# Performance work log

Hardware: AMD Instinct MI355X
Metric: run time of the kernel (lower is better)

## Reference

```python
import jax, jax.numpy as jnp
import numpy as np

LAM = 1.0
N_ITERS = 20
TOL = 1e-6


def setup_inputs() -> dict:
    key = jax.random.key(0)
    k0, k1, k2, k3, k4 = jax.random.split(key, 5)
    B, M, d, E, a = 8, 50000, 8, 800000, 8
    c0 = jax.random.normal(k0, (B, M, d), dtype=jnp.float32)
    src = jax.random.randint(k1, (E,), 0, M, dtype=jnp.int32)
    dst = jax.random.randint(k2, (E,), 0, M, dtype=jnp.int32)
    R_src = jax.random.normal(k3, (E, a, d), dtype=jnp.float32)
    R_dst = jax.random.normal(k4, (E, a, d), dtype=jnp.float32)
    return {"c0": c0, "src": src, "dst": dst, "R_src": R_src, "R_dst": R_dst}


def _batch_dot(x, y):
    # [B,M,d] x [B,M,d] -> [B,1,1]
    return jnp.sum(x * y, axis=(1, 2), keepdims=True)


def _matvec(p, src, dst, R_src, R_dst):
    # p: [B,M,d] -> p + lam * L p via per-edge gather-einsum-scatter
    r = (jnp.einsum('ead,bed->bea', R_src, p[:, src, :])
         - jnp.einsum('ead,bed->bea', R_dst, p[:, dst, :]))  # [B,E,a]
    c_src = jnp.einsum('ead,bea->bed', R_src, r)   # [B,E,d]
    c_dst = -jnp.einsum('ead,bea->bed', R_dst, r)  # [B,E,d]
    acc = jnp.zeros_like(p).at[:, src, :].add(c_src).at[:, dst, :].add(c_dst)
    return p + LAM * acc


def _cg_solve(b, x0, src, dst, R_src, R_dst):
    mv = lambda q: _matvec(q, src, dst, R_src, R_dst)
    x = x0
    r = b - mv(x)
    p = r
    rsold = _batch_dot(r, r)
    done = jnp.array(False)

    def body(i, state):
        x, r, p, rsold, done = state
        Ap = mv(p)
        alpha = rsold / (_batch_dot(p, Ap) + 1e-12)
        x_new = x + alpha * p
        r_new = r - alpha * Ap
        rsnew = _batch_dot(r_new, r_new)
        conv = jnp.sqrt(jnp.mean(rsnew)) < TOL  # torch breaks AFTER updating x,r
        p_new = r_new + rsnew / (rsold + 1e-12) * p
        x = jnp.where(done, x, x_new)
        r = jnp.where(done, r, r_new)
        frozen = done | conv
        p = jnp.where(frozen, p, p_new)
        rsold = jnp.where(frozen, rsold, rsnew)
        return (x, r, p, rsold, frozen)

    x, _, _, _, _ = jax.lax.fori_loop(0, N_ITERS, body, (x, r, p, rsold, done))
    return x


def reference(c0, src, dst, R_src, R_dst):
    c0_f = c0.astype(jnp.float32)
    c = _cg_solve(c0_f, c0_f, src, dst, R_src, R_dst)
    return c.astype(c0.dtype)
```

## Files before the change

kernel.cpp:

```cpp
#include <hip/hip_runtime.h>
#include <math.h>

constexpr float LAM = 1.0f;
constexpr int   NIT = 20;
constexpr float TOL = 1e-6f;

typedef float f4 __attribute__((ext_vector_type(4)));

#define S_RSOLD 0
#define S_ALPHA 8
#define S_BETA  16
#define S_FLAG  24
#define S_PAP   32
#define S_RS    (32+2048)
#define SCAL_F  (32+4096)

__device__ __forceinline__ float dot8v(f4 a0, f4 a1, f4 b0, f4 b1){
  return a0[0]*b0[0] + a0[1]*b0[1] + a0[2]*b0[2] + a0[3]*b0[3]
       + a1[0]*b1[0] + a1[1]*b1[1] + a1[2]*b1[2] + a1[3]*b1[3];
}

__global__ void k_setup_nm(float* __restrict__ scal, int* __restrict__ cursor, int Mn){
  int i = blockIdx.x * blockDim.x + threadIdx.x;
  int stride = gridDim.x * blockDim.x;
  for (int j = i; j < SCAL_F; j += stride) scal[j] = 0.f;
  for (int j = i; j < Mn; j += stride) cursor[j] = 0;
}

__global__ void k_deg(const int* __restrict__ src, const int* __restrict__ dst,
                      int* __restrict__ cnt, int E){
  int i = blockIdx.x * blockDim.x + threadIdx.x;
  int stride = gridDim.x * blockDim.x;
  for (int e = i; e < E; e += stride){
    atomicAdd(&cnt[src[e]], 1);
    atomicAdd(&cnt[dst[e]], 1);
  }
}

__global__ void k_scan(int* __restrict__ cnt, int* __restrict__ rowptr,
                       int* __restrict__ cursor, int Mn, int tot){
  __shared__ int sm[1024];
  const int T = 1024;
  int t = threadIdx.x;
  int chunk = (Mn + T - 1) / T;
  int lo = t * chunk, hi = lo + chunk; if (hi > Mn) hi = Mn;
  int s = 0;
  for (int i = lo; i < hi; ++i) s += cnt[i];
  sm[t] = s;
  __syncthreads();
  for (int o = 1; o < T; o <<= 1){
    int v = (t >= o) ? sm[t - o] : 0;
    __syncthreads();
    sm[t] += v;
    __syncthreads();
  }
  int base = (t == 0) ? 0 : sm[t - 1];
  for (int i = lo; i < hi; ++i){
    int c = cnt[i];
    rowptr[i] = base;
    cursor[i] = base;
    base += c;
  }
  if (t == T - 1) rowptr[Mn] = tot;
}

__global__ void k_fill(const int* __restrict__ src, const int* __restrict__ dst,
                       int* __restrict__ cursor, int* __restrict__ col,
                       int* __restrict__ es, int E){
  int i = blockIdx.x * blockDim.x + threadIdx.x;
  int stride = gridDim.x * blockDim.x;
  for (int e = i; e < E; e += stride){
    int s = src[e], t = dst[e];
    int ps = atomicAdd(&cursor[s], 1);
    col[ps] = t; es[ps] = (e << 1);
    int pt = atomicAdd(&cursor[t], 1);
    col[pt] = s; es[pt] = (e << 1) | 1;
  }
}

__global__ void k_medge(const float* __restrict__ Rs, const float* __restrict__ Rd,
                        float* __restrict__ Mb, int E){
  int g  = blockIdx.x * blockDim.x + threadIdx.x;
  int wv = g >> 6, l = g & 63;
  int nw = (gridDim.x * blockDim.x) >> 6;
  int d1 = l >> 3, d2 = l & 7;
  for (int e = wv; e < E; e += nw){
    float rs = Rs[(size_t)e * 64 + l];
    float rd = Rd[(size_t)e * 64 + l];
    float Mm = 0.f;
    #pragma unroll
    for (int a = 0; a < 8; ++a)
      Mm += __shfl(rs, a * 8 + d1, 64) * __shfl(rd, a * 8 + d2, 64);
    Mb[(size_t)e * 64 + l] = Mm;
  }
}

__global__ void k_buildd(const float* __restrict__ Rs, const float* __restrict__ Rd,
                         const int* __restrict__ rowptr, const int* __restrict__ es,
                         float* __restrict__ Dd, int v0, int v1){
  int g = blockIdx.x * blockDim.x + threadIdx.x;
  int v = v0 + (g >> 6);
  if (v >= v1) return;
  int l = g & 63, d1 = l >> 3, d2 = l & 7;
  float Dacc = 0.f;
  int j0 = rowptr[v], j1 = rowptr[v + 1];
  int j = j0;
  for (; j + 2 <= j1; j += 2){
    int e0 = es[j], e1 = es[j + 1];
    const float* R0 = (e0 & 1) ? Rd : Rs;
    const float* R1 = (e1 & 1) ? Rd : Rs;
    float x0 = R0[(size_t)(e0 >> 1) * 64 + l];
    float x1 = R1[(size_t)(e1 >> 1) * 64 + l];
    #pragma unroll
    for (int a = 0; a < 8; ++a){
      float p0 = __shfl(x0, a * 8 + d1, 64);
      float s0 = __shfl(x0, a * 8 + d2, 64);
      float p1 = __shfl(x1, a * 8 + d1, 64);
      float s1 = __shfl(x1, a * 8 + d2, 64);
      Dacc += p0 * s0 + p1 * s1;
    }
  }
  for (; j < j1; ++j){
    int e0 = es[j];
    const float* R0 = (e0 & 1) ? Rd : Rs;
    float x0 = R0[(size_t)(e0 >> 1) * 64 + l];
    #pragma unroll
    for (int a = 0; a < 8; ++a)
      Dacc += __shfl(x0, a * 8 + d1, 64) * __shfl(x0, a * 8 + d2, 64);
  }
  Dd[(size_t)v * 64 + l] = ((d1 == d2) ? 1.f : 0.f) + LAM * Dacc;
}

__global__ void k_mv(const float* __restrict__ Mb, const float* __restrict__ Dd,
                     const int* __restrict__ rowptr, const int* __restrict__ col,
                     const int* __restrict__ es, const float* __restrict__ p,
                     float* __restrict__ out, float* __restrict__ scal, int Mn){
  if (*(const int*)(scal + S_FLAG)) return;
  __shared__ float pbuf[4][2][8][64];
  __shared__ float mbuf[4][2][8][64];
  __shared__ int   cbuf[4][128];
  __shared__ int   ebuf[4][128];
  int g = blockIdx.x * blockDim.x + threadIdx.x;
  int v = g >> 6;
  bool active = (v < Mn);
  int w  = threadIdx.x >> 6;
  int l  = g & 63;
  int hi = l >> 3, lo = l & 7;
  int k8 = lo * 8;
  int b8 = hi * 8;
  int j0 = 0, j1 = 0, rowlen = 0;
  if (active){
    j0 = rowptr[v]; j1 = rowptr[v + 1];
    rowlen = j1 - j0;
    for (int jj = l; jj < rowlen && jj < 128; jj += 64){
      cbuf[w][jj] = col[j0 + jj];
      ebuf[w][jj] = es[j0 + jj];
    }
  }
  __syncthreads();
  if (!active) return;

  int nch = (rowlen + 7) >> 3;

  auto gather = [&](int n, f4& gp0, f4& gp1, f4& gm0, f4& gm1){
    int jj = n * 8 + hi;
    int c = v, e = 0;
    if (jj < rowlen){
      if (jj < 128){ c = cbuf[w][jj]; e = ebuf[w][jj] >> 1; }
      else         { c = col[j0 + jj]; e = es[j0 + jj] >> 1; }
    }
    const float* pc = p + (size_t)c * 64 + k8;
    gp0 = *(const f4*)pc;
    gp1 = *(const f4*)(pc + 4);
    const float* mc = Mb + (size_t)e * 64 + k8;
    gm0 = *(const f4*)mc;
    gm1 = *(const f4*)(mc + 4);
  };

  const f4* pv4 = (const f4*)(p + (size_t)v * 64 + b8);
  f4 pv0 = pv4[0], pv1 = pv4[1];
  const f4* dr4 = (const f4*)(Dd + (size_t)v * 64 + k8);
  float acc = dot8v(dr4[0], dr4[1], pv0, pv1);

  if (nch > 0){
    f4 u0, u1, m0, m1;
    gather(0, u0, u1, m0, m1);
    float* dp = &pbuf[w][0][hi][k8];
    *(f4*)dp = u0; *(f4*)(dp + 4) = u1;
    float* dm = &mbuf[w][0][hi][k8];
    *(f4*)dm = m0; *(f4*)(dm + 4) = m1;
  }

  for (int n = 0; n < nch; ++n){
    int nb = n & 1;
    bool more = (n + 1 < nch);
    f4 gp0, gp1, gm0, gm1;
    if (more) gather(n + 1, gp0, gp1, gm0, gm1);
    int jb = n * 8;
    int lim = rowlen - jb;
    #pragma unroll
    for (int q = 0; q < 8; ++q){
      if (q < lim){
        int jj = jb + q;
        int sd = ((jj < 128) ? ebuf[w][jj] : es[j0 + jj]) & 1;
        const float* pr = &pbuf[w][nb][q][b8];
        f4 q0 = *(const f4*)pr, q1 = *(const f4*)(pr + 4);
        const float* mc = &mbuf[w][nb][q][0];
        if (!sd){
          f4 m0 = *(const f4*)(mc + k8);
          f4 m1 = *(const f4*)(mc + k8 + 4);
          acc -= LAM * dot8v(m0, m1, q0, q1);
        } else {
          acc -= LAM * ( mc[lo]      * q0[0] + mc[lo +  8] * q0[1]
                       + mc[lo + 16] * q0[2] + mc[lo + 24] * q0[3]
                       + mc[lo + 32] * q1[0] + mc[lo + 40] * q1[1]
                       + mc[lo + 48] * q1[2] + mc[lo + 56] * q1[3]);
        }
      }
    }
    if (more){
      float* dp = &pbuf[w][nb ^ 1][hi][k8];
      *(f4*)dp = gp0; *(f4*)(dp + 4) = gp1;
      float* dm = &mbuf[w][nb ^ 1][hi][k8];
      *(f4*)dm = gm0; *(f4*)(dm + 4) = gm1;
    }
  }
  out[(size_t)v * 64 + l] = acc;
  float pself = (lo & 4) ? ((lo & 2) ? ((lo & 1) ? pv1[3] : pv1[2])
                                     : ((lo & 1) ? pv1[1] : pv1[0]))
                         : ((lo & 2) ? ((lo & 1) ? pv0[3] : pv0[2])
                                     : ((lo & 1) ? pv0[1] : pv0[0]));
  float part = pself * acc;
  part += __shfl_xor(part, 1, 64);
  part += __shfl_xor(part, 2, 64);
  part += __shfl_xor(part, 4, 64);
  if (lo == 0)
    atomicAdd(&scal[S_PAP + hi * 256 + (blockIdx.x & 255)], part);
}

__global__ void k_perm(const float* __restrict__ c0, float* __restrict__ xp, int Mn){
  int i = blockIdx.x * blockDim.x + threadIdx.x;
  int n4 = Mn * 16;
  if (i >= n4) return;
  int v = i >> 4, rem = i & 15, b = rem >> 1, half = rem & 1;
  f4 cv = *(const f4*)(c0 + ((size_t)b * Mn + v) * 8 + half * 4);
  ((f4*)xp)[i] = cv;
}

__global__ void k_init_nm(float* __restrict__ p, const float* __restrict__ Ap,
                          float* __restrict__ r, float* __restrict__ x_bm,
                          float* __restrict__ scal, int n4tot, int Mn){
  int i = blockIdx.x * blockDim.x + threadIdx.x;
  int l = threadIdx.x & 63;
  float part = 0.f;
  if (i < n4tot){
    f4 cv = ((const f4*)p)[i];
    f4 av = ((const f4*)Ap)[i];
    f4 rv = cv - av;
    ((f4*)r)[i] = rv;
    ((f4*)p)[i] = rv;
    int v = i >> 4, rem = i & 15, b = rem >> 1, half = rem & 1;
    ((f4*)x_bm)[((size_t)b * Mn + v) * 2 + half] = cv;
    part = rv[0]*rv[0] + rv[1]*rv[1] + rv[2]*rv[2] + rv[3]*rv[3];
  }
  part += __shfl_xor(part, 1, 64);
  part += __shfl_xor(part, 16, 64);
  part += __shfl_xor(part, 32, 64);
  if ((l & 49) == 0)
    atomicAdd(&scal[S_RS + ((l >> 1) & 7) * 256 + (blockIdx.x & 255)], part);
}

__global__ void k_s0(float* __restrict__ scal){
  __shared__ float sm[256];
  int t = threadIdx.x;
  int b = t >> 5, k0 = t & 31;
  float s = 0.f;
  #pragma unroll
  for (int i = 0; i < 8; ++i) s += scal[S_RS + b * 256 + k0 + i * 32];
  sm[t] = s;
  __syncthreads();
  if (t < 8){
    float tot = 0.f;
    #pragma unroll
    for (int i = 0; i < 32; ++i) tot += sm[t * 32 + i];
    scal[S_RSOLD + t] = tot;
  }
  __syncthreads();
  for (int i = t; i < 4096; i += 256) scal[S_PAP + i] = 0.f;
}

__global__ void k_alpha(float* __restrict__ scal){
  if (*(const int*)(scal + S_FLAG)) return;
  __shared__ float sm[256];
  int t = threadIdx.x;
  int b = t >> 5, k0 = t & 31;
  float s = 0.f;
  #pragma unroll
  for (int i = 0; i < 8; ++i) s += scal[S_PAP + b * 256 + k0 + i * 32];
  sm[t] = s;
  __syncthreads();
  if (t < 8){
    float tot = 0.f;
    #pragma unroll
    for (int i = 0; i < 32; ++i) tot += sm[t * 32 + i];
    scal[S_ALPHA + t] = scal[S_RSOLD + t] / (tot + 1e-12f);
  }
}

__global__ void k_upd_nm(float* __restrict__ x_bm, float* __restrict__ r,
                         const float* __restrict__ p, const float* __restrict__ Ap,
                         float* __restrict__ scal, int n4tot, int Mn){
  if (*(const int*)(scal + S_FLAG)) return;
  int i = blockIdx.x * blockDim.x + threadIdx.x;
  int l = threadIdx.x & 63;
  float part = 0.f;
  if (i < n4tot){
    int v = i >> 4, rem = i & 15, b = rem >> 1, half = rem & 1;
    float al = scal[S_ALPHA + b];
    size_t xi = ((size_t)b * Mn + v) * 2 + half;
    f4 pv = ((const f4*)p)[i];
    f4 av = ((const f4*)Ap)[i];
    f4 xv = ((f4*)x_bm)[xi];
    f4 rv = ((f4*)r)[i];
    xv += al * pv;
    rv -= al * av;
    ((f4*)x_bm)[xi] = xv;
    ((f4*)r)[i] = rv;
    part = rv[0]*rv[0] + rv[1]*rv[1] + rv[2]*rv[2] + rv[3]*rv[3];
  }
  part += __shfl_xor(part, 1, 64);
  part += __shfl_xor(part, 16, 64);
  part += __shfl_xor(part, 32, 64);
  if ((l & 49) == 0)
    atomicAdd(&scal[S_RS + ((l >> 1) & 7) * 256 + (blockIdx.x & 255)], part);
}

__global__ void k_s2(float* __restrict__ scal){
  if (*(const int*)(scal + S_FLAG)) return;
  __shared__ float sm[256];
  __shared__ float rsn[8];
  int t = threadIdx.x;
  int b = t >> 5, k0 = t & 31;
  float s = 0.f;
  #pragma unroll
  for (int i = 0; i < 8; ++i) s += scal[S_RS + b * 256 + k0 + i * 32];
  sm[t] = s;
  __syncthreads();
  if (t < 8){
    float tot = 0.f;
    #pragma unroll
    for (int i = 0; i < 32; ++i) tot += sm[t * 32 + i];
    rsn[t] = tot;
  }
  __syncthreads();
  if (t == 0){
    float ssum = 0.f;
    for (int bb = 0; bb < 8; ++bb) ssum += rsn[bb];
    if (sqrtf(ssum / 8.0f) < TOL){
      *(int*)(scal + S_FLAG) = 1;
    } else {
      for (int bb = 0; bb < 8; ++bb){
        scal[S_BETA + bb]  = rsn[bb] / (scal[S_RSOLD + bb] + 1e-12f);
        scal[S_RSOLD + bb] = rsn[bb];
      }
    }
  }
  __syncthreads();
  for (int i = t; i < 4096; i += 256) scal[S_PAP + i] = 0.f;
}

__global__ void k_pupd_nm(const float* __restrict__ r, float* __restrict__ p,
                          const float* __restrict__ scal, int n4tot){
  if (*(const int*)(scal + S_FLAG)) return;
  int i = blockIdx.x * blockDim.x + threadIdx.x;
  if (i >= n4tot) return;
  int b = (i >> 1) & 7;
  float be = scal[S_BETA + b];
  f4 rv = ((const f4*)r)[i];
  f4 pv = ((f4*)p)[i];
  pv = rv + be * pv;
  ((f4*)p)[i] = pv;
}

#define OS_RSOLD 0
#define OS_PAP   8
#define OS_RSNEW 16
#define OS_ALPHA 24
#define OS_BETA  32
#define OS_FLAG  40

__device__ __forceinline__ float blk_reduce_256(float v){
  __shared__ float sm[4];
  #pragma unroll
  for (int o = 32; o > 0; o >>= 1) v += __shfl_down(v, o, 64);
  int lane = threadIdx.x & 63, w = threadIdx.x >> 6;
  if (lane == 0) sm[w] = v;
  __syncthreads();
  return (threadIdx.x == 0) ? (sm[0] + sm[1] + sm[2] + sm[3]) : 0.f;
}

__global__ void k_setup_fb(float* scal){
  int i = blockIdx.x * blockDim.x + threadIdx.x;
  if (i < 64) scal[i] = 0.f;
}

__global__ void k_apinit(const float* __restrict__ in, float* __restrict__ out,
                         int n4tot, const int* __restrict__ flag){
  if (*flag) return;
  int j = blockIdx.x * blockDim.x + threadIdx.x;
  if (j < n4tot) ((f4*)out)[j] = ((const f4*)in)[j];
}

__global__ void k_mv_edge_fb(const float* __restrict__ Rs, const float* __restrict__ Rd,
                             const int* __restrict__ src, const int* __restrict__ dst,
                             const float* __restrict__ in, float* __restrict__ out,
                             int Mn, int E, const int* __restrict__ flag){
  if (*flag) return;
  int g  = blockIdx.x * blockDim.x + threadIdx.x;
  int wv = g >> 6, l = g & 63;
  int nw = (gridDim.x * blockDim.x) >> 6;
  int b = l >> 3, q = l & 7;
  for (int e = wv; e < E; e += nw){
    int s = src[e], t = dst[e];
    const f4* rs4 = (const f4*)(Rs + (size_t)e * 64 + q * 8);
    const f4* rd4 = (const f4*)(Rd + (size_t)e * 64 + q * 8);
    const f4* ps4 = (const f4*)(in + ((size_t)b * Mn + s) * 8);
    const f4* pd4 = (const f4*)(in + ((size_t)b * Mn + t) * 8);
    f4 ra0 = rs4[0], ra1 = rs4[1], pa0 = ps4[0], pa1 = ps4[1];
    f4 rb0 = rd4[0], rb1 = rd4[1], pb0 = pd4[0], pb1 = pd4[1];
    float re = dot8v(ra0, ra1, pa0, pa1) - dot8v(rb0, rb1, pb0, pb1);
    float cs = 0.f, cd = 0.f;
    #pragma unroll
    for (int a = 0; a < 8; ++a){
      float rea = __shfl(re, b * 8 + a, 64);
      cs += Rs[(size_t)e * 64 + a * 8 + q] * rea;
      cd += Rd[(size_t)e * 64 + a * 8 + q] * rea;
    }
    atomicAdd(&out[((size_t)b * Mn + s) * 8 + q],  LAM * cs);
    atomicAdd(&out[((size_t)b * Mn + t) * 8 + q], -LAM * cd);
  }
}

__global__ void k_init_o(const float* __restrict__ c0, const float* __restrict__ Ap,
                         float* __restrict__ x, float* __restrict__ r, float* __restrict__ p,
                         float* scal, int n4){
  int b = blockIdx.y;
  size_t base = (size_t)b * n4;
  int j = blockIdx.x * blockDim.x + threadIdx.x;
  float part = 0.f;
  if (j < n4){
    f4 cv = ((const f4*)c0)[base + j];
    f4 av = ((const f4*)Ap)[base + j];
    f4 rv = cv - av;
    ((f4*)x)[base + j] = cv;
    ((f4*)r)[base + j] = rv;
    ((f4*)p)[base + j] = rv;
    part = rv[0]*rv[0] + rv[1]*rv[1] + rv[2]*rv[2] + rv[3]*rv[3];
  }
  float tot = blk_reduce_256(part);
  if (threadIdx.x == 0) atomicAdd(&scal[OS_RSOLD + b], tot);
}

__global__ void k_dot_o(const float* __restrict__ p, const float* __restrict__ Ap,
                        float* scal, int n4){
  const int* flag = (const int*)(scal + OS_FLAG);
  if (*flag) return;
  int b = blockIdx.y;
  size_t base = (size_t)b * n4;
  int j = blockIdx.x * blockDim.x + threadIdx.x;
  float part = 0.f;
  if (j < n4){
    f4 pv = ((const f4*)p)[base + j];
    f4 av = ((const f4*)Ap)[base + j];
    part = pv[0]*av[0] + pv[1]*av[1] + pv[2]*av[2] + pv[3]*av[3];
  }
  float tot = blk_reduce_256(part);
  if (threadIdx.x == 0) atomicAdd(&scal[OS_PAP + b], tot);
}

__global__ void k_s1_o(float* scal){
  const int* flag = (const int*)(scal + OS_FLAG);
  if (*flag) return;
  int t = threadIdx.x;
  if (t < 8){
    scal[OS_ALPHA + t] = scal[OS_RSOLD + t] / (scal[OS_PAP + t] + 1e-12f);
    scal[OS_RSNEW + t] = 0.f;
  }
}

__global__ void k_upd_o(float* __restrict__ x, float* __restrict__ r,
                        const float* __restrict__ p, const float* __restrict__ Ap,
                        float* scal, int n4){
  const int* flag = (const int*)(scal + OS_FLAG);
  if (*flag) return;
  int b = blockIdx.y;
  size_t base = (size_t)b * n4;
  float al = scal[OS_ALPHA + b];
  int j = blockIdx.x * blockDim.x + threadIdx.x;
  float part = 0.f;
  if (j < n4){
    f4 pv = ((const f4*)p)[base + j];
    f4 av = ((const f4*)Ap)[base + j];
    f4 xv = ((f4*)x)[base + j];
    f4 rv = ((f4*)r)[base + j];
    xv += al * pv;
    rv -= al * av;
    ((f4*)x)[base + j] = xv;
    ((f4*)r)[base + j] = rv;
    part = rv[0]*rv[0] + rv[1]*rv[1] + rv[2]*rv[2] + rv[3]*rv[3];
  }
  float tot = blk_reduce_256(part);
  if (threadIdx.x == 0) atomicAdd(&scal[OS_RSNEW + b], tot);
}

__global__ void k_s2_o(float* scal){
  int* flag = (int*)(scal + OS_FLAG);
  if (*flag) return;
  if (threadIdx.x == 0){
    float ssum = 0.f;
    for (int bb = 0; bb < 8; ++bb) ssum += scal[OS_RSNEW + bb];
    if (sqrtf(ssum / 8.0f) < TOL){
      *flag = 1;
    } else {
      for (int bb = 0; bb < 8; ++bb){
        scal[OS_BETA + bb]  = scal[OS_RSNEW + bb] / (scal[OS_RSOLD + bb] + 1e-12f);
        scal[OS_RSOLD + bb] = scal[OS_RSNEW + bb];
        scal[OS_PAP + bb]   = 0.f;
      }
    }
  }
}

__global__ void k_pupd_o(const float* __restrict__ r, float* __restrict__ p,
                         float* scal, int n4){
  const int* flag = (const int*)(scal + OS_FLAG);
  if (*flag) return;
  int b = blockIdx.y;
  size_t base = (size_t)b * n4;
  float be = scal[OS_BETA + b];
  int j = blockIdx.x * blockDim.x + threadIdx.x;
  if (j < n4){
    f4 rv = ((const f4*)r)[base + j];
    f4 pv = ((f4*)p)[base + j];
    pv = rv + be * pv;
    ((f4*)p)[base + j] = pv;
  }
}

extern "C" void kernel_launch(void* const* d_in, const int* in_sizes, int n_in,
                              void* d_out, int out_size, void* d_ws, size_t ws_size,
                              hipStream_t stream){
  const float* c0  = (const float*)d_in[0];
  const int*   src = (const int*)d_in[1];
  const int*   dst = (const int*)d_in[2];
  const float* Rs  = (const float*)d_in[3];
  const float* Rd  = (const float*)d_in[4];

  int N  = in_sizes[0];
  int Mn = N / 64;
  int E  = in_sizes[1];
  int n4tot = N / 4;
  int twoE = 2 * E;

  float* ws = (float*)d_ws;
  size_t off = 0;
  float* r    = ws + off;  off += N;
  float* p    = ws + off;  off += N;
  float* Ap   = ws + off;  off += N;
  float* scal = ws + off;  off += SCAL_F;
  float* Dd   = ws + off;  off += (size_t)Mn * 64;
  int* rowptr = (int*)(ws + off);  off += (size_t)((Mn + 1 + 3) & ~3);
  int* cursor = (int*)(ws + off);  off += (size_t)((Mn + 3) & ~3);
  int* colA   = (int*)(ws + off);  off += (size_t)twoE;
  int* esA    = (int*)(ws + off);  off += (size_t)twoE;
  float* Mb   = ws + off;  off += (size_t)E * 64;
  size_t need_main = off * 4;

  int nb_vec  = (n4tot + 255) / 256;
  int nb_node = (Mn * 64 + 255) / 256;

  if (ws_size >= need_main){
    k_setup_nm<<<512, 256, 0, stream>>>(scal, cursor, Mn);
    k_deg  <<<1024, 256, 0, stream>>>(src, dst, cursor, E);
    k_scan <<<1, 1024, 0, stream>>>(cursor, rowptr, cursor, Mn, twoE);
    k_fill <<<1024, 256, 0, stream>>>(src, dst, cursor, colA, esA, E);
    k_medge<<<4096, 256, 0, stream>>>(Rs, Rd, Mb, E);
    int Mh = (Mn + 1) / 2;
    int nb_h1 = (Mh * 64 + 255) / 256;
    int nb_h2 = ((Mn - Mh) * 64 + 255) / 256;
    k_buildd<<<nb_h1, 256, 0, stream>>>(Rs, Rd, rowptr, esA, Dd, 0, Mh);
    k_buildd<<<nb_h2, 256, 0, stream>>>(Rs, Rd, rowptr, esA, Dd, Mh, Mn);

    float* x_bm = (float*)d_out;
    k_perm<<<nb_vec, 256, 0, stream>>>(c0, p, Mn);
    k_mv<<<nb_node, 256, 0, stream>>>(Mb, Dd, rowptr, colA, esA, p, Ap, scal, Mn);
    k_init_nm<<<nb_vec, 256, 0, stream>>>(p, Ap, r, x_bm, scal, n4tot, Mn);
    k_s0<<<1, 256, 0, stream>>>(scal);

    for (int it = 0; it < NIT; ++it){
      k_mv<<<nb_node, 256, 0, stream>>>(Mb, Dd, rowptr, colA, esA, p, Ap, scal, Mn);
      k_alpha<<<1, 256, 0, stream>>>(scal);
      k_upd_nm<<<nb_vec, 256, 0, stream>>>(x_bm, r, p, Ap, scal, n4tot, Mn);
      k_s2<<<1, 256, 0, stream>>>(scal);
      k_pupd_nm<<<nb_vec, 256, 0, stream>>>(r, p, scal, n4tot);
    }
  } else {
    float* fr    = ws;
    float* fp    = fr + N;
    float* fAp   = fp + N;
    float* fscal = fAp + N;
    const int* flagp = (const int*)(fscal + OS_FLAG);
    int n4 = Mn * 2;
    dim3 vgrid((n4 + 255) / 256, 8);
    int cb = (n4tot + 255) / 256;
    float* x = (float*)d_out;

    k_setup_fb<<<1, 64, 0, stream>>>(fscal);
    k_apinit<<<cb, 256, 0, stream>>>(c0, fAp, n4tot, flagp);
    k_mv_edge_fb<<<2048, 256, 0, stream>>>(Rs, Rd, src, dst, c0, fAp, Mn, E, flagp);
    k_init_o<<<vgrid, 256, 0, stream>>>(c0, fAp, x, fr, fp, fscal, n4);
    for (int it = 0; it < NIT; ++it){
      k_apinit<<<cb, 256, 0, stream>>>(fp, fAp, n4tot, flagp);
      k_mv_edge_fb<<<2048, 256, 0, stream>>>(Rs, Rd, src, dst, fp, fAp, Mn, E, flagp);
      k_dot_o<<<vgrid, 256, 0, stream>>>(fp, fAp, fscal, n4);
      k_s1_o<<<1, 64, 0, stream>>>(fscal);
      k_upd_o<<<vgrid, 256, 0, stream>>>(x, fr, fp, fAp, fscal, n4);
      k_s2_o<<<1, 64, 0, stream>>>(fscal);
      k_pupd_o<<<vgrid, 256, 0, stream>>>(fr, fp, fscal, n4);
    }
  }
}
```

Baseline: 5.145 ms.

## Fold alpha reduction into update kernel and single-buffer padded SpMV gather tiles

The separate single-block alpha kernel is removed. Each update block now redundantly reduces the 256 partial p·Ap sums per batch into shared memory, which saves one launch per CG iteration. The SpMV kernel drops its double-buffered shared staging for one padded buffer per wave. It also removes the block-wide __syncthreads, relying on wave-local lockstep, and adds a fast path with no bounds check for full 8-edge chunks. The risks are redundant per-block reduction work and correctness that depends on implicit wave synchronisation.

```diff
diff --git a/kernel.cpp b/kernel.cpp
--- a/kernel.cpp
+++ b/kernel.cpp
@@ -136,45 +136,35 @@
                      const int* __restrict__ es, const float* __restrict__ p,
                      float* __restrict__ out, float* __restrict__ scal, int Mn){
   if (*(const int*)(scal + S_FLAG)) return;
-  __shared__ float pbuf[4][2][8][64];
-  __shared__ float mbuf[4][2][8][64];
+  __shared__ float pbuf[4][8][68];
+  __shared__ float mbuf[4][8][68];
   __shared__ int   cbuf[4][128];
   __shared__ int   ebuf[4][128];
   int g = blockIdx.x * blockDim.x + threadIdx.x;
   int v = g >> 6;
-  bool active = (v < Mn);
+  if (v >= Mn) return;
   int w  = threadIdx.x >> 6;
   int l  = g & 63;
   int hi = l >> 3, lo = l & 7;
   int k8 = lo * 8;
   int b8 = hi * 8;
-  int j0 = 0, j1 = 0, rowlen = 0;
-  if (active){
-    j0 = rowptr[v]; j1 = rowptr[v + 1];
-    rowlen = j1 - j0;
-    for (int jj = l; jj < rowlen && jj < 128; jj += 64){
-      cbuf[w][jj] = col[j0 + jj];
-      ebuf[w][jj] = es[j0 + jj];
-    }
-  }
-  __syncthreads();
-  if (!active) return;
+  int j0 = rowptr[v];
+  int rowlen = rowptr[v + 1] - j0;
+
+  for (int jj = l; jj < rowlen && jj < 128; jj += 64){
+    cbuf[w][jj] = col[j0 + jj];
+    ebuf[w][jj] = es[j0 + jj];
+  }
 
   int nch = (rowlen + 7) >> 3;
 
-  auto gather = [&](int n, f4& gp0, f4& gp1, f4& gm0, f4& gm1){
+  auto gaddr = [&](int n, int& c, int& e){
     int jj = n * 8 + hi;
-    int c = v, e = 0;
+    c = v; e = 0;
     if (jj < rowlen){
       if (jj < 128){ c = cbuf[w][jj]; e = ebuf[w][jj] >> 1; }
       else         { c = col[j0 + jj]; e = es[j0 + jj] >> 1; }
     }
-    const float* pc = p + (size_t)c * 64 + k8;
-    gp0 = *(const f4*)pc;
-    gp1 = *(const f4*)(pc + 4);
-    const float* mc = Mb + (size_t)e * 64 + k8;
-    gm0 = *(const f4*)mc;
-    gm1 = *(const f4*)(mc + 4);
   };
 
   const f4* pv4 = (const f4*)(p + (size_t)v * 64 + b8);
@@ -182,30 +172,38 @@
   const f4* dr4 = (const f4*)(Dd + (size_t)v * 64 + k8);
   float acc = dot8v(dr4[0], dr4[1], pv0, pv1);
 
+  f4 gp0, gp1, gm0, gm1;
   if (nch > 0){
-    f4 u0, u1, m0, m1;
-    gather(0, u0, u1, m0, m1);
-    float* dp = &pbuf[w][0][hi][k8];
-    *(f4*)dp = u0; *(f4*)(dp + 4) = u1;
-    float* dm = &mbuf[w][0][hi][k8];
-    *(f4*)dm = m0; *(f4*)(dm + 4) = m1;
+    int c, e; gaddr(0, c, e);
+    const float* pc = p + (size_t)c * 64 + k8;
+    gp0 = *(const f4*)pc; gp1 = *(const f4*)(pc + 4);
+    const float* mc = Mb + (size_t)e * 64 + k8;
+    gm0 = *(const f4*)mc; gm1 = *(const f4*)(mc + 4);
   }
 
   for (int n = 0; n < nch; ++n){
-    int nb = n & 1;
+    float* dp = &pbuf[w][hi][k8];
+    *(f4*)dp = gp0; *(f4*)(dp + 4) = gp1;
+    float* dm = &mbuf[w][hi][k8];
+    *(f4*)dm = gm0; *(f4*)(dm + 4) = gm1;
     bool more = (n + 1 < nch);
-    f4 gp0, gp1, gm0, gm1;
-    if (more) gather(n + 1, gp0, gp1, gm0, gm1);
+    if (more){
+      int c, e; gaddr(n + 1, c, e);
+      const float* pc = p + (size_t)c * 64 + k8;
+      gp0 = *(const f4*)pc; gp1 = *(const f4*)(pc + 4);
+      const float* mc = Mb + (size_t)e * 64 + k8;
+      gm0 = *(const f4*)mc; gm1 = *(const f4*)(mc + 4);
+    }
     int jb = n * 8;
     int lim = rowlen - jb;
-    #pragma unroll
-    for (int q = 0; q < 8; ++q){
-      if (q < lim){
+    if (lim >= 8){
+      #pragma unroll
+      for (int q = 0; q < 8; ++q){
         int jj = jb + q;
         int sd = ((jj < 128) ? ebuf[w][jj] : es[j0 + jj]) & 1;
-        const float* pr = &pbuf[w][nb][q][b8];
+        const float* pr = &pbuf[w][q][b8];
         f4 q0 = *(const f4*)pr, q1 = *(const f4*)(pr + 4);
-        const float* mc = &mbuf[w][nb][q][0];
+        const float* mc = &mbuf[w][q][0];
         if (!sd){
           f4 m0 = *(const f4*)(mc + k8);
           f4 m1 = *(const f4*)(mc + k8 + 4);
@@ -217,12 +215,27 @@
                        + mc[lo + 48] * q1[2] + mc[lo + 56] * q1[3]);
         }
       }
-    }
-    if (more){
-      float* dp = &pbuf[w][nb ^ 1][hi][k8];
-      *(f4*)dp = gp0; *(f4*)(dp + 4) = gp1;
-      float* dm = &mbuf[w][nb ^ 1][hi][k8];
-      *(f4*)dm = gm0; *(f4*)(dm + 4) = gm1;
+    } else {
+      #pragma unroll
+      for (int q = 0; q < 8; ++q){
+        if (q < lim){
+          int jj = jb + q;
+          int sd = ((jj < 128) ? ebuf[w][jj] : es[j0 + jj]) & 1;
+          const float* pr = &pbuf[w][q][b8];
+          f4 q0 = *(const f4*)pr, q1 = *(const f4*)(pr + 4);
+          const float* mc = &mbuf[w][q][0];
+          if (!sd){
+            f4 m0 = *(const f4*)(mc + k8);
+            f4 m1 = *(const f4*)(mc + k8 + 4);
+            acc -= LAM * dot8v(m0, m1, q0, q1);
+          } else {
+            acc -= LAM * ( mc[lo]      * q0[0] + mc[lo +  8] * q0[1]
+                         + mc[lo + 16] * q0[2] + mc[lo + 24] * q0[3]
+                         + mc[lo + 32] * q1[0] + mc[lo + 40] * q1[1]
+                         + mc[lo + 48] * q1[2] + mc[lo + 56] * q1[3]);
+          }
+        }
+      }
     }
   }
   out[(size_t)v * 64 + l] = acc;
@@ -289,34 +302,26 @@
   for (int i = t; i < 4096; i += 256) scal[S_PAP + i] = 0.f;
 }
 
-__global__ void k_alpha(float* __restrict__ scal){
-  if (*(const int*)(scal + S_FLAG)) return;
-  __shared__ float sm[256];
-  int t = threadIdx.x;
-  int b = t >> 5, k0 = t & 31;
-  float s = 0.f;
-  #pragma unroll
-  for (int i = 0; i < 8; ++i) s += scal[S_PAP + b * 256 + k0 + i * 32];
-  sm[t] = s;
-  __syncthreads();
-  if (t < 8){
-    float tot = 0.f;
-    #pragma unroll
-    for (int i = 0; i < 32; ++i) tot += sm[t * 32 + i];
-    scal[S_ALPHA + t] = scal[S_RSOLD + t] / (tot + 1e-12f);
-  }
-}
-
 __global__ void k_upd_nm(float* __restrict__ x_bm, float* __restrict__ r,
                          const float* __restrict__ p, const float* __restrict__ Ap,
                          float* __restrict__ scal, int n4tot, int Mn){
   if (*(const int*)(scal + S_FLAG)) return;
-  int i = blockIdx.x * blockDim.x + threadIdx.x;
-  int l = threadIdx.x & 63;
+  __shared__ float sal[8];
+  int t = threadIdx.x;
+  if (t < 8){
+    float s = 0.f;
+    const float* pp = scal + S_PAP + t * 256;
+    #pragma unroll 4
+    for (int k = 0; k < 256; ++k) s += pp[k];
+    sal[t] = scal[S_RSOLD + t] / (s + 1e-12f);
+  }
+  __syncthreads();
+  int i = blockIdx.x * blockDim.x + t;
+  int l = t & 63;
   float part = 0.f;
   if (i < n4tot){
     int v = i >> 4, rem = i & 15, b = rem >> 1, half = rem & 1;
-    float al = scal[S_ALPHA + b];
+    float al = sal[b];
     size_t xi = ((size_t)b * Mn + v) * 2 + half;
     f4 pv = ((const f4*)p)[i];
     f4 av = ((const f4*)Ap)[i];
@@ -599,7 +604,6 @@
 
     for (int it = 0; it < NIT; ++it){
       k_mv<<<nb_node, 256, 0, stream>>>(Mb, Dd, rowptr, colA, esA, p, Ap, scal, Mn);
-      k_alpha<<<1, 256, 0, stream>>>(scal);
       k_upd_nm<<<nb_vec, 256, 0, stream>>>(x_bm, r, p, Ap, scal, n4tot, Mn);
       k_s2<<<1, 256, 0, stream>>>(scal);
       k_pupd_nm<<<nb_vec, 256, 0, stream>>>(r, p, scal, n4tot);
```

Measured after the change: 5.086 ms. About the same (-1.1%).
